# Optimization experiments

Measured on AMD Instinct MI355X. Metric: run time of the kernel, lower is better.

## Reference

```python
import jax, jax.numpy as jnp
import numpy as np

DIM = 768
HEADS = 12
HIDDEN = 3072  # int(dim * 4.0)
EPS = 1e-5


def layernorm(x, g, b):
    mu = jnp.mean(x, axis=-1, keepdims=True)
    var = jnp.mean(jnp.square(x - mu), axis=-1, keepdims=True)
    return (x - mu) * jax.lax.rsqrt(var + EPS) * g + b


def setup_inputs() -> dict:
    key = jax.random.key(0)
    ks = jax.random.split(key, 8)
    s = 0.02
    return {
        "x": jax.random.normal(ks[0], (16, 1024, DIM), dtype=jnp.float32),
        "ln1_g": jnp.ones((DIM,), jnp.float32),
        "ln1_b": jnp.zeros((DIM,), jnp.float32),
        "qkv_w": jax.random.normal(ks[1], (3 * DIM, DIM), jnp.float32) * s,  # torch Linear weight [out,in], no bias (qkv_bias=False)
        "proj_w": jax.random.normal(ks[2], (DIM, DIM), jnp.float32) * s,
        "proj_b": jnp.zeros((DIM,), jnp.float32),
        "ln2_g": jnp.ones((DIM,), jnp.float32),
        "ln2_b": jnp.zeros((DIM,), jnp.float32),
        "fc1_w": jax.random.normal(ks[3], (HIDDEN, DIM), jnp.float32) * s,
        "fc1_b": jnp.zeros((HIDDEN,), jnp.float32),
        "fc2_w": jax.random.normal(ks[4], (DIM, HIDDEN), jnp.float32) * s,
        "fc2_b": jnp.zeros((DIM,), jnp.float32),
    }


def block(x, ln1_g, ln1_b, qkv_w, proj_w, proj_b, ln2_g, ln2_b, fc1_w, fc1_b, fc2_w, fc2_b):
    B, N, C = x.shape
    hd = C // HEADS
    scale = hd ** -0.5
    # --- attention branch ---
    h = layernorm(x, ln1_g, ln1_b)
    qkv = h @ qkv_w.T                                   # [B,N,3C]
    qkv = qkv.reshape(B, N, 3, HEADS, hd)
    q, k, v = jnp.moveaxis(qkv, 2, 0)                   # each [B,N,H,hd]
    q = q.transpose(0, 2, 1, 3)                          # [B,H,N,hd]
    k = k.transpose(0, 2, 1, 3)
    v = v.transpose(0, 2, 1, 3)
    attn = jnp.einsum('bhqd,bhkd->bhqk', q, k) * scale   # [B,H,N,N]
    attn = jax.nn.softmax(attn, axis=-1)
    o = jnp.einsum('bhqk,bhkd->bhqd', attn, v)           # [B,H,N,hd]
    o = o.transpose(0, 2, 1, 3).reshape(B, N, C)
    x = x + o @ proj_w.T + proj_b
    # --- mlp branch ---
    h = layernorm(x, ln2_g, ln2_b)
    h = jax.nn.gelu(h @ fc1_w.T + fc1_b, approximate=False)
    x = x + h @ fc2_w.T + fc2_b
    return x


def reference(x, ln1_g, ln1_b, qkv_w, proj_w, proj_b, ln2_g, ln2_b, fc1_w, fc1_b, fc2_w, fc2_b):
    return block(x, ln1_g, ln1_b, qkv_w, proj_w, proj_b, ln2_g, ln2_b, fc1_w, fc1_b, fc2_w, fc2_b)
```

## Files before the change

### kernel.cpp

```cpp
#include <hip/hip_runtime.h>
#include <cstdint>
#include <cstddef>

typedef __attribute__((ext_vector_type(8))) short short8;
typedef __attribute__((ext_vector_type(4))) float f32x4;
typedef __attribute__((ext_vector_type(4))) unsigned short us4;

#define GAS(p) ((const __attribute__((address_space(1))) void*)(p))
#define LAS(p) ((__attribute__((address_space(3))) void*)(p))

__device__ __forceinline__ unsigned short f2bf(float f) {
  union { float f; unsigned u; } v; v.f = f;
  return (unsigned short)((v.u + 0x7fffu + ((v.u >> 16) & 1u)) >> 16);
}

__global__ __launch_bounds__(256) void cvt_kernel(const float* __restrict__ in,
                                                  unsigned short* __restrict__ out, int n4) {
  int i = blockIdx.x * 256 + threadIdx.x;
  if (i >= n4) return;
  f32x4 v = ((const f32x4*)in)[i];
  us4 o;
#pragma unroll
  for (int j = 0; j < 4; ++j) o[j] = f2bf(v[j]);
  ((us4*)out)[i] = o;
}

__global__ __launch_bounds__(256) void ln_kernel(const float* __restrict__ x,
                                                 const float* __restrict__ g,
                                                 const float* __restrict__ b,
                                                 unsigned short* __restrict__ out) {
  const int wave = threadIdx.x >> 6, lane = threadIdx.x & 63;
  const int row = blockIdx.x * 4 + wave;
  const float* xr = x + (size_t)row * 768;
  f32x4 v[3];
  float s = 0.f, sq = 0.f;
#pragma unroll
  for (int c = 0; c < 3; ++c) {
    v[c] = *(const f32x4*)(xr + c * 256 + lane * 4);
#pragma unroll
    for (int j = 0; j < 4; ++j) { s += v[c][j]; sq += v[c][j] * v[c][j]; }
  }
#pragma unroll
  for (int off = 32; off > 0; off >>= 1) { s += __shfl_xor(s, off); sq += __shfl_xor(sq, off); }
  const float mu = s * (1.f / 768.f);
  const float var = sq * (1.f / 768.f) - mu * mu;
  const float rs = rsqrtf(var + 1e-5f);
  unsigned short* orow = out + (size_t)row * 768;
#pragma unroll
  for (int c = 0; c < 3; ++c) {
    f32x4 gg = *(const f32x4*)(g + c * 256 + lane * 4);
    f32x4 bb = *(const f32x4*)(b + c * 256 + lane * 4);
    us4 o;
#pragma unroll
    for (int j = 0; j < 4; ++j) o[j] = f2bf((v[c][j] - mu) * rs * gg[j] + bb[j]);
    *(us4*)(orow + c * 256 + lane * 4) = o;
  }
}

template <int EPI, int NN, int K>
__global__ __launch_bounds__(1024, 4) void gemmW(
    const unsigned short* __restrict__ A, const unsigned short* __restrict__ W,
    float* __restrict__ outF, const float* __restrict__ bias, const float* __restrict__ res,
    unsigned short* __restrict__ outU,
    unsigned short* __restrict__ q, unsigned short* __restrict__ kk, unsigned short* __restrict__ vt) {
  __shared__ unsigned short As[4][8192];
  __shared__ unsigned short Bs[4][8192];
  const int tid = threadIdx.x;
  const int wave = tid >> 6, lane = tid & 63;
  const int lr = lane & 15, lg = lane >> 4;
  const int wr = wave >> 2, wc = wave & 3;
  constexpr int GX = NN / 256;
  constexpr int NWG = GX * 64;
  int id = blockIdx.y * GX + blockIdx.x;
  id = (id & 7) * (NWG / 8) + (id >> 3);
  const int row0 = (id / GX) * 256, col0 = (id % GX) * 256;
  f32x4 acc[4][4] = {};
  const int sc = ((tid & 3) ^ ((tid >> 3) & 3)) * 8;
  const unsigned short* ag = A + (size_t)(row0 + (tid >> 2)) * K + sc;
  const unsigned short* bg = W + (size_t)(col0 + (tid >> 2)) * K + sc;
  const int rsw = (lg ^ ((lr >> 1) & 3)) << 4;
  constexpr int KT = K / 32;

#define STG(buf, t_)                                                                           \
  {                                                                                            \
    __builtin_amdgcn_global_load_lds(GAS(ag + (t_) * 32), LAS(&As[buf][wave * 512]), 16, 0, 0);\
    __builtin_amdgcn_global_load_lds(GAS(bg + (t_) * 32), LAS(&Bs[buf][wave * 512]), 16, 0, 0);\
  }

#define TILE(buf, t_)                                                                          \
  {                                                                                            \
    if ((t_) < KT - 2)       { asm volatile("s_waitcnt vmcnt(4)" ::: "memory"); }              \
    else if ((t_) == KT - 2) { asm volatile("s_waitcnt vmcnt(2)" ::: "memory"); }              \
    else                     { asm volatile("s_waitcnt vmcnt(0)" ::: "memory"); }              \
    __builtin_amdgcn_s_barrier();                                                              \
    if ((t_) + 3 < KT) STG(((buf) + 3) & 3, (t_) + 3);                                         \
    const char* Ab = (const char*)As + (buf) * 16384;                                          \
    const char* Bb = (const char*)Bs + (buf) * 16384;                                          \
    short8 af[4], bfv[4];                                                                      \
    _Pragma("unroll")                                                                          \
    for (int m = 0; m < 4; ++m) {                                                              \
      const int arow = wr * 64 + m * 16 + lr;                                                  \
      af[m] = *(const short8*)(Ab + arow * 64 + rsw);                                          \
    }                                                                                          \
    _Pragma("unroll")                                                                          \
    for (int n = 0; n < 4; ++n) {                                                              \
      const int brow = wc * 64 + n * 16 + lr;                                                  \
      bfv[n] = *(const short8*)(Bb + brow * 64 + rsw);                                         \
    }                                                                                          \
    __builtin_amdgcn_s_setprio(1);                                                             \
    _Pragma("unroll")                                                                          \
    for (int m = 0; m < 4; ++m)                                                                \
      _Pragma("unroll")                                                                        \
      for (int n = 0; n < 4; ++n)                                                              \
        acc[m][n] = __builtin_amdgcn_mfma_f32_16x16x32_bf16(af[m], bfv[n], acc[m][n], 0, 0, 0);\
    __builtin_amdgcn_s_setprio(0);                                                             \
  }

  STG(0, 0);
  STG(1, 1);
  STG(2, 2);
  for (int tt = 0; tt < KT; tt += 4) {
    TILE(0, tt);
    TILE(1, tt + 1);
    TILE(2, tt + 2);
    TILE(3, tt + 3);
  }
#undef TILE
#undef STG

  if (EPI == 0) {
    const int s = (col0 >= 1536) ? 2 : (col0 >= 768 ? 1 : 0);
    const int hh = (col0 + wc * 64 - s * 768) >> 6;
#pragma unroll
    for (int m = 0; m < 4; ++m)
#pragma unroll
      for (int n = 0; n < 4; ++n) {
        const int d = n * 16 + lr;
        const int g0 = row0 + wr * 64 + m * 16 + lg * 4;
        const int bt = g0 >> 10, nt0 = g0 & 1023;
        const size_t bh = (size_t)(bt * 12 + hh);
        if (s == 2) {
          us4 o;
#pragma unroll
          for (int r = 0; r < 4; ++r) o[r] = f2bf(acc[m][n][r]);
          *(us4*)(vt + (bh * 64 + d) * 1024 + nt0) = o;
        } else {
#pragma unroll
          for (int r = 0; r < 4; ++r) {
            const float val = acc[m][n][r];
            if (s == 0) q[(bh * 1024 + nt0 + r) * 64 + d] = f2bf(val * 0.18033688f);
            else        kk[(bh * 1024 + nt0 + r) * 64 + d] = f2bf(val);
          }
        }
      }
  } else if (EPI == 1) {
#pragma unroll
    for (int m = 0; m < 4; ++m)
#pragma unroll
      for (int n = 0; n < 4; ++n) {
        const int gcol = col0 + wc * 64 + n * 16 + lr;
        const float bn = bias[gcol];
#pragma unroll
        for (int r = 0; r < 4; ++r) {
          const int grow = row0 + wr * 64 + m * 16 + lg * 4 + r;
          const size_t idx = (size_t)grow * NN + gcol;
          outF[idx] = acc[m][n][r] + bn + res[idx];
        }
      }
  } else {
#pragma unroll
    for (int m = 0; m < 4; ++m)
#pragma unroll
      for (int n = 0; n < 4; ++n) {
        const int gcol = col0 + wc * 64 + n * 16 + lr;
        const float bn = bias[gcol];
#pragma unroll
        for (int r = 0; r < 4; ++r) {
          const int grow = row0 + wr * 64 + m * 16 + lg * 4 + r;
          const size_t idx = (size_t)grow * NN + gcol;
          const float t = acc[m][n][r] + bn;
          const float u = t * (1.59576912f + t * t * 0.07135481f);
          const float eu = __expf(-u);
          outU[idx] = f2bf(t / (1.f + eu));
        }
      }
  }
}

__global__ __launch_bounds__(256) void attn_kernel(
    const unsigned short* __restrict__ Q, const unsigned short* __restrict__ K,
    const unsigned short* __restrict__ V, unsigned short* __restrict__ O) {
  __shared__ unsigned short Ks[2][64 * 64];
  __shared__ unsigned short Vs[2][64 * 64];
  __shared__ unsigned short Ps[4][32 * 64];
  const int tid = threadIdx.x, wave = tid >> 6, lane = tid & 63;
  const int lr = lane & 15, lg = lane >> 4;
  const int id = blockIdx.x;
  const int qt = (id >> 3) & 7;
  const int head = (id & 7) + 8 * (id >> 6);
  const int hh = head % 12, bb = head / 12;
  const size_t bh = (size_t)bb * 12 + hh;
  const unsigned short* Qg = Q + bh * 1024 * 64;
  const unsigned short* Kg = K + bh * 1024 * 64;
  const unsigned short* Vg = V + bh * 64 * 1024;
  const int q0 = qt * 128 + wave * 32;
  short8 aq[2][2];
#pragma unroll
  for (int nq = 0; nq < 2; ++nq)
#pragma unroll
    for (int kb = 0; kb < 2; ++kb)
      aq[nq][kb] = *(const short8*)(Qg + (size_t)(q0 + nq * 16 + lr) * 64 + kb * 32 + lg * 8);
  float m_run[2] = {-1e30f, -1e30f}, l_run[2] = {0.f, 0.f};
  f32x4 oacc[4][2] = {};
  const int srow = tid >> 3;
  const int sswz = (((tid & 7) * 16) ^ ((srow & 7) << 4)) >> 1;
  char* Pw = (char*)&Ps[wave][0];

#define ATTN_STAGE(buf, t_)                                                                      \
  {                                                                                              \
    const int kv_ = (t_) * 64;                                                                   \
    _Pragma("unroll")                                                                            \
    for (int is = 0; is < 2; ++is) {                                                             \
      __builtin_amdgcn_global_load_lds(GAS(Kg + (size_t)(kv_ + is * 32 + srow) * 64 + sswz),     \
                                       LAS(&Ks[buf][is * 2048 + wave * 512]), 16, 0, 0);         \
      __builtin_amdgcn_global_load_lds(GAS(Vg + (size_t)(is * 32 + srow) * 1024 + kv_ + sswz),   \
                                       LAS(&Vs[buf][is * 2048 + wave * 512]), 16, 0, 0);         \
    }                                                                                            \
  }

#define ATILE(cur, t_)                                                                           \
  {                                                                                              \
    if ((t_) < 15) { asm volatile("s_waitcnt vmcnt(4)" ::: "memory"); }                          \
    else           { asm volatile("s_waitcnt vmcnt(0)" ::: "memory"); }                          \
    __builtin_amdgcn_s_barrier();                                                                \
    __builtin_amdgcn_sched_barrier(0);                                                           \
    f32x4 sacc[4][2] = {};                                                                       \
    _Pragma("unroll")                                                                            \
    for (int kb = 0; kb < 2; ++kb) {                                                             \
      short8 kf[4];                                                                              \
      _Pragma("unroll")                                                                          \
      for (int mk = 0; mk < 4; ++mk) {                                                           \
        const int row = mk * 16 + lr;                                                            \
        const int boff = row * 128 + ((kb * 64 + lg * 16) ^ ((row & 7) << 4));                   \
        kf[mk] = *(const short8*)((const char*)&Ks[cur][0] + boff);                              \
      }                                                                                          \
      _Pragma("unroll")                                                                          \
      for (int mk = 0; mk < 4; ++mk)                                                             \
        _Pragma("unroll")                                                                        \
        for (int nq = 0; nq < 2; ++nq)                                                           \
          sacc[mk][nq] = __builtin_amdgcn_mfma_f32_16x16x32_bf16(kf[mk], aq[nq][kb], sacc[mk][nq], 0, 0, 0); \
    }                                                                                            \
    _Pragma("unroll")                                                                            \
    for (int nq = 0; nq < 2; ++nq) {                                                             \
      float mx = fmaxf(fmaxf(sacc[0][nq][0], sacc[0][nq][1]), fmaxf(sacc[0][nq][2], sacc[0][nq][3])); \
      _Pragma("unroll")                                                                          \
      for (int mk = 1; mk < 4; ++mk)                                                             \
        mx = fmaxf(mx, fmaxf(fmaxf(sacc[mk][nq][0], sacc[mk][nq][1]), fmaxf(sacc[mk][nq][2], sacc[mk][nq][3]))); \
      mx = fmaxf(mx, __shfl_xor(mx, 16));                                                        \
      mx = fmaxf(mx, __shfl_xor(mx, 32));                                                        \
      if (!__all(mx - m_run[nq] <= 8.f)) {                                                       \
        const float mnew = fmaxf(m_run[nq], mx);                                                 \
        const float alpha = exp2f(m_run[nq] - mnew);                                             \
        l_run[nq] *= alpha;                                                                      \
        _Pragma("unroll")                                                                        \
        for (int mb = 0; mb < 4; ++mb)                                                           \
          _Pragma("unroll")                                                                      \
          for (int r = 0; r < 4; ++r) oacc[mb][nq][r] *= alpha;                                  \
        m_run[nq] = mnew;                                                                        \
      }                                                                                          \
      float ssum = 0.f;                                                                          \
      _Pragma("unroll")                                                                          \
      for (int mk = 0; mk < 4; ++mk)                                                             \
        _Pragma("unroll")                                                                        \
        for (int r = 0; r < 4; ++r) {                                                            \
          const float p = exp2f(sacc[mk][nq][r] - m_run[nq]);                                    \
          sacc[mk][nq][r] = p;                                                                   \
          ssum += p;                                                                             \
        }                                                                                        \
      ssum += __shfl_xor(ssum, 16);                                                              \
      ssum += __shfl_xor(ssum, 32);                                                              \
      l_run[nq] += ssum;                                                                         \
      const int prow = nq * 16 + lr;                                                             \
      _Pragma("unroll")                                                                          \
      for (int mk = 0; mk < 4; ++mk) {                                                           \
        unsigned p0, p1;                                                                         \
        asm("v_cvt_pk_bf16_f32 %0, %1, %2" : "=v"(p0) : "v"(sacc[mk][nq][0]), "v"(sacc[mk][nq][1])); \
        asm("v_cvt_pk_bf16_f32 %0, %1, %2" : "=v"(p1) : "v"(sacc[mk][nq][2]), "v"(sacc[mk][nq][3])); \
        uint2 w; w.x = p0; w.y = p1;                                                             \
        *(uint2*)(Pw + prow * 128 + ((mk * 32 + lg * 8) ^ ((lr & 7) << 4))) = w;                 \
      }                                                                                          \
    }                                                                                            \
    _Pragma("unroll")                                                                            \
    for (int kb = 0; kb < 2; ++kb) {                                                             \
      short8 vf[4];                                                                              \
      _Pragma("unroll")                                                                          \
      for (int mb = 0; mb < 4; ++mb) {                                                           \
        const int row = mb * 16 + lr;                                                            \
        const int boff = row * 128 + ((kb * 64 + lg * 16) ^ ((row & 7) << 4));                   \
        vf[mb] = *(const short8*)((const char*)&Vs[cur][0] + boff);                              \
      }                                                                                          \
      _Pragma("unroll")                                                                          \
      for (int nq = 0; nq < 2; ++nq) {                                                           \
        const int prow = nq * 16 + lr;                                                           \
        const short8 pb = *(const short8*)(Pw + prow * 128 + ((kb * 64 + lg * 16) ^ ((lr & 7) << 4))); \
        _Pragma("unroll")                                                                        \
        for (int mb = 0; mb < 4; ++mb)                                                           \
          oacc[mb][nq] = __builtin_amdgcn_mfma_f32_16x16x32_bf16(vf[mb], pb, oacc[mb][nq], 0, 0, 0); \
      }                                                                                          \
    }                                                                                            \
    asm volatile("s_waitcnt lgkmcnt(0)" ::: "memory");                                           \
    __builtin_amdgcn_sched_barrier(0);                                                           \
    __builtin_amdgcn_s_barrier();                                                                \
    if ((t_) + 2 < 16) ATTN_STAGE(cur, (t_) + 2);                                                \
  }

  ATTN_STAGE(0, 0);
  ATTN_STAGE(1, 1);
  for (int tt = 0; tt < 8; ++tt) {
    ATILE(0, 2 * tt)
    ATILE(1, 2 * tt + 1)
  }
#undef ATILE
#undef ATTN_STAGE
#pragma unroll
  for (int nq = 0; nq < 2; ++nq) {
    const float linv = 1.f / l_run[nq];
    const size_t tok = (size_t)(bb << 10) + q0 + nq * 16 + lr;
#pragma unroll
    for (int mb = 0; mb < 4; ++mb) {
      us4 o;
#pragma unroll
      for (int r = 0; r < 4; ++r) o[r] = f2bf(oacc[mb][nq][r] * linv);
      *(us4*)(O + tok * 768 + hh * 64 + mb * 16 + lg * 4) = o;
    }
  }
}

extern "C" void kernel_launch(void* const* d_in, const int* in_sizes, int n_in,
                              void* d_out, int out_size, void* d_ws, size_t ws_size,
                              hipStream_t stream) {
  const float* x      = (const float*)d_in[0];
  const float* ln1_g  = (const float*)d_in[1];
  const float* ln1_b  = (const float*)d_in[2];
  const float* qkv_w  = (const float*)d_in[3];
  const float* proj_w = (const float*)d_in[4];
  const float* proj_b = (const float*)d_in[5];
  const float* ln2_g  = (const float*)d_in[6];
  const float* ln2_b  = (const float*)d_in[7];
  const float* fc1_w  = (const float*)d_in[8];
  const float* fc1_b  = (const float*)d_in[9];
  const float* fc2_w  = (const float*)d_in[10];
  const float* fc2_b  = (const float*)d_in[11];
  float* out = (float*)d_out;
  char* ws = (char*)d_ws;

  unsigned short* wqkv = (unsigned short*)(ws + 0);
  unsigned short* wproj = (unsigned short*)(ws + 3538944);
  unsigned short* wfc1 = (unsigned short*)(ws + 4718592);
  unsigned short* wfc2 = (unsigned short*)(ws + 9437184);
  unsigned short* hbuf = (unsigned short*)(ws + 14155776);
  char* big = ws + 39321600;
  unsigned short* qb  = (unsigned short*)(big);
  unsigned short* kb  = (unsigned short*)(big + 25165824);
  unsigned short* vtb = (unsigned short*)(big + 50331648);
  unsigned short* ob  = (unsigned short*)(big + 75497472);
  unsigned short* hid = (unsigned short*)(big);

  cvt_kernel<<<1728, 256, 0, stream>>>(qkv_w, wqkv, 442368);
  cvt_kernel<<<576, 256, 0, stream>>>(proj_w, wproj, 147456);
  cvt_kernel<<<2304, 256, 0, stream>>>(fc1_w, wfc1, 589824);
  cvt_kernel<<<2304, 256, 0, stream>>>(fc2_w, wfc2, 589824);

  ln_kernel<<<4096, 256, 0, stream>>>(x, ln1_g, ln1_b, hbuf);
  gemmW<0, 2304, 768><<<dim3(9, 64), 1024, 0, stream>>>(
      hbuf, wqkv, nullptr, nullptr, nullptr, nullptr, qb, kb, vtb);
  attn_kernel<<<dim3(1536), 256, 0, stream>>>(qb, kb, vtb, ob);
  gemmW<1, 768, 768><<<dim3(3, 64), 1024, 0, stream>>>(
      ob, wproj, out, proj_b, x, nullptr, nullptr, nullptr, nullptr);
  ln_kernel<<<4096, 256, 0, stream>>>(out, ln2_g, ln2_b, hbuf);
  gemmW<2, 3072, 768><<<dim3(12, 64), 1024, 0, stream>>>(
      hbuf, wfc1, nullptr, fc1_b, nullptr, hid, nullptr, nullptr, nullptr);
  gemmW<1, 768, 3072><<<dim3(3, 64), 1024, 0, stream>>>(
      hid, wfc2, out, fc2_b, out, nullptr, nullptr, nullptr, nullptr);
}
```

Before: 462.6 us.

## Parameterize GEMM tile width and compute softmax row sums via MFMA

The GEMM kernel gets a templated N-tile width (BN). The QKV, proj and fc2 GEMMs switch to 192-wide tiles, giving more workgroups (768 or 256 instead of 576 or 192) for better CU fill on the 256-CU part, and the B-tile load wraps rows when BN<256. In attention, the per-row exp-sum with cross-lane shuffles is replaced by an extra MFMA against a vector of bf16 ones, and the max reduction is restructured into a chain. The cost is an extra MFMA per block, and the bf16-rounded P now also feeds the denominator, which slightly changes numerics.

```diff
diff --git a/kernel.cpp b/kernel.cpp
--- a/kernel.cpp
+++ b/kernel.cpp
@@ -57,34 +57,38 @@
   }
 }
 
-template <int EPI, int NN, int K>
+template <int EPI, int NN, int K, int BN>
 __global__ __launch_bounds__(1024, 4) void gemmW(
     const unsigned short* __restrict__ A, const unsigned short* __restrict__ W,
     float* __restrict__ outF, const float* __restrict__ bias, const float* __restrict__ res,
     unsigned short* __restrict__ outU,
     unsigned short* __restrict__ q, unsigned short* __restrict__ kk, unsigned short* __restrict__ vt) {
+  constexpr int NFR = BN / 64;
+  constexpr int BW = BN >> 4;
   __shared__ unsigned short As[4][8192];
-  __shared__ unsigned short Bs[4][8192];
+  __shared__ unsigned short Bs[4][BN * 32];
   const int tid = threadIdx.x;
   const int wave = tid >> 6, lane = tid & 63;
   const int lr = lane & 15, lg = lane >> 4;
   const int wr = wave >> 2, wc = wave & 3;
-  constexpr int GX = NN / 256;
+  constexpr int GX = NN / BN;
   constexpr int NWG = GX * 64;
   int id = blockIdx.y * GX + blockIdx.x;
   id = (id & 7) * (NWG / 8) + (id >> 3);
-  const int row0 = (id / GX) * 256, col0 = (id % GX) * 256;
-  f32x4 acc[4][4] = {};
+  const int row0 = (id / GX) * 256, col0 = (id % GX) * BN;
+  f32x4 acc[4][NFR] = {};
   const int sc = ((tid & 3) ^ ((tid >> 3) & 3)) * 8;
+  int br = tid >> 2; if (br >= BN) br -= BN;
   const unsigned short* ag = A + (size_t)(row0 + (tid >> 2)) * K + sc;
-  const unsigned short* bg = W + (size_t)(col0 + (tid >> 2)) * K + sc;
+  const unsigned short* bg = W + (size_t)(col0 + br) * K + sc;
+  const int bwav = (wave < BW ? wave : wave - BW) * 512;
   const int rsw = (lg ^ ((lr >> 1) & 3)) << 4;
   constexpr int KT = K / 32;
 
 #define STG(buf, t_)                                                                           \
   {                                                                                            \
     __builtin_amdgcn_global_load_lds(GAS(ag + (t_) * 32), LAS(&As[buf][wave * 512]), 16, 0, 0);\
-    __builtin_amdgcn_global_load_lds(GAS(bg + (t_) * 32), LAS(&Bs[buf][wave * 512]), 16, 0, 0);\
+    __builtin_amdgcn_global_load_lds(GAS(bg + (t_) * 32), LAS(&Bs[buf][bwav]), 16, 0, 0);      \
   }
 
 #define TILE(buf, t_)                                                                          \
@@ -95,23 +99,23 @@
     __builtin_amdgcn_s_barrier();                                                              \
     if ((t_) + 3 < KT) STG(((buf) + 3) & 3, (t_) + 3);                                         \
     const char* Ab = (const char*)As + (buf) * 16384;                                          \
-    const char* Bb = (const char*)Bs + (buf) * 16384;                                          \
-    short8 af[4], bfv[4];                                                                      \
+    const char* Bb = (const char*)&Bs[buf][0];                                                 \
+    short8 af[4], bfv[NFR];                                                                    \
     _Pragma("unroll")                                                                          \
     for (int m = 0; m < 4; ++m) {                                                              \
       const int arow = wr * 64 + m * 16 + lr;                                                  \
       af[m] = *(const short8*)(Ab + arow * 64 + rsw);                                          \
     }                                                                                          \
     _Pragma("unroll")                                                                          \
-    for (int n = 0; n < 4; ++n) {                                                              \
-      const int brow = wc * 64 + n * 16 + lr;                                                  \
+    for (int n = 0; n < NFR; ++n) {                                                            \
+      const int brow = wc * (NFR * 16) + n * 16 + lr;                                          \
       bfv[n] = *(const short8*)(Bb + brow * 64 + rsw);                                         \
     }                                                                                          \
     __builtin_amdgcn_s_setprio(1);                                                             \
     _Pragma("unroll")                                                                          \
     for (int m = 0; m < 4; ++m)                                                                \
       _Pragma("unroll")                                                                        \
-      for (int n = 0; n < 4; ++n)                                                              \
+      for (int n = 0; n < NFR; ++n)                                                            \
         acc[m][n] = __builtin_amdgcn_mfma_f32_16x16x32_bf16(af[m], bfv[n], acc[m][n], 0, 0, 0);\
     __builtin_amdgcn_s_setprio(0);                                                             \
   }
@@ -130,12 +134,13 @@
 
   if (EPI == 0) {
     const int s = (col0 >= 1536) ? 2 : (col0 >= 768 ? 1 : 0);
-    const int hh = (col0 + wc * 64 - s * 768) >> 6;
 #pragma unroll
     for (int m = 0; m < 4; ++m)
 #pragma unroll
-      for (int n = 0; n < 4; ++n) {
-        const int d = n * 16 + lr;
+      for (int n = 0; n < NFR; ++n) {
+        const int gb = col0 - s * 768 + wc * (NFR * 16) + n * 16;
+        const int hh = gb >> 6;
+        const int d = (gb & 63) + lr;
         const int g0 = row0 + wr * 64 + m * 16 + lg * 4;
         const int bt = g0 >> 10, nt0 = g0 & 1023;
         const size_t bh = (size_t)(bt * 12 + hh);
@@ -157,8 +162,8 @@
 #pragma unroll
     for (int m = 0; m < 4; ++m)
 #pragma unroll
-      for (int n = 0; n < 4; ++n) {
-        const int gcol = col0 + wc * 64 + n * 16 + lr;
+      for (int n = 0; n < NFR; ++n) {
+        const int gcol = col0 + wc * (NFR * 16) + n * 16 + lr;
         const float bn = bias[gcol];
 #pragma unroll
         for (int r = 0; r < 4; ++r) {
@@ -171,8 +176,8 @@
 #pragma unroll
     for (int m = 0; m < 4; ++m)
 #pragma unroll
-      for (int n = 0; n < 4; ++n) {
-        const int gcol = col0 + wc * 64 + n * 16 + lr;
+      for (int n = 0; n < NFR; ++n) {
+        const int gcol = col0 + wc * (NFR * 16) + n * 16 + lr;
         const float bn = bias[gcol];
 #pragma unroll
         for (int r = 0; r < 4; ++r) {
@@ -210,8 +215,12 @@
 #pragma unroll
     for (int kb = 0; kb < 2; ++kb)
       aq[nq][kb] = *(const short8*)(Qg + (size_t)(q0 + nq * 16 + lr) * 64 + kb * 32 + lg * 8);
-  float m_run[2] = {-1e30f, -1e30f}, l_run[2] = {0.f, 0.f};
+  float m_run[2] = {-1e30f, -1e30f};
   f32x4 oacc[4][2] = {};
+  f32x4 accl[2] = {};
+  short8 vones;
+#pragma unroll
+  for (int j = 0; j < 8; ++j) vones[j] = (short)0x3F80;
   const int srow = tid >> 3;
   const int sswz = (((tid & 7) * 16) ^ ((srow & 7) << 4)) >> 1;
   char* Pw = (char*)&Ps[wave][0];
@@ -252,34 +261,31 @@
     }                                                                                            \
     _Pragma("unroll")                                                                            \
     for (int nq = 0; nq < 2; ++nq) {                                                             \
-      float mx = fmaxf(fmaxf(sacc[0][nq][0], sacc[0][nq][1]), fmaxf(sacc[0][nq][2], sacc[0][nq][3])); \
-      _Pragma("unroll")                                                                          \
-      for (int mk = 1; mk < 4; ++mk)                                                             \
-        mx = fmaxf(mx, fmaxf(fmaxf(sacc[mk][nq][0], sacc[mk][nq][1]), fmaxf(sacc[mk][nq][2], sacc[mk][nq][3]))); \
+      float mx = fmaxf(fmaxf(sacc[0][nq][0], sacc[0][nq][1]), sacc[0][nq][2]);                   \
+      mx = fmaxf(fmaxf(mx, sacc[0][nq][3]), sacc[1][nq][0]);                                     \
+      mx = fmaxf(fmaxf(mx, sacc[1][nq][1]), sacc[1][nq][2]);                                     \
+      mx = fmaxf(fmaxf(mx, sacc[1][nq][3]), sacc[2][nq][0]);                                     \
+      mx = fmaxf(fmaxf(mx, sacc[2][nq][1]), sacc[2][nq][2]);                                     \
+      mx = fmaxf(fmaxf(mx, sacc[2][nq][3]), sacc[3][nq][0]);                                     \
+      mx = fmaxf(fmaxf(mx, sacc[3][nq][1]), sacc[3][nq][2]);                                     \
+      mx = fmaxf(mx, sacc[3][nq][3]);                                                            \
       mx = fmaxf(mx, __shfl_xor(mx, 16));                                                        \
       mx = fmaxf(mx, __shfl_xor(mx, 32));                                                        \
       if (!__all(mx - m_run[nq] <= 8.f)) {                                                       \
         const float mnew = fmaxf(m_run[nq], mx);                                                 \
         const float alpha = exp2f(m_run[nq] - mnew);                                             \
-        l_run[nq] *= alpha;                                                                      \
+        accl[nq][0] *= alpha; accl[nq][1] *= alpha; accl[nq][2] *= alpha; accl[nq][3] *= alpha;  \
         _Pragma("unroll")                                                                        \
         for (int mb = 0; mb < 4; ++mb)                                                           \
           _Pragma("unroll")                                                                      \
           for (int r = 0; r < 4; ++r) oacc[mb][nq][r] *= alpha;                                  \
         m_run[nq] = mnew;                                                                        \
       }                                                                                          \
-      float ssum = 0.f;                                                                          \
       _Pragma("unroll")                                                                          \
       for (int mk = 0; mk < 4; ++mk)                                                             \
         _Pragma("unroll")                                                                        \
-        for (int r = 0; r < 4; ++r) {                                                            \
-          const float p = exp2f(sacc[mk][nq][r] - m_run[nq]);                                    \
-          sacc[mk][nq][r] = p;                                                                   \
-          ssum += p;                                                                             \
-        }                                                                                        \
-      ssum += __shfl_xor(ssum, 16);                                                              \
-      ssum += __shfl_xor(ssum, 32);                                                              \
-      l_run[nq] += ssum;                                                                         \
+        for (int r = 0; r < 4; ++r)                                                              \
+          sacc[mk][nq][r] = exp2f(sacc[mk][nq][r] - m_run[nq]);                                  \
       const int prow = nq * 16 + lr;                                                             \
       _Pragma("unroll")                                                                          \
       for (int mk = 0; mk < 4; ++mk) {                                                           \
@@ -303,6 +309,7 @@
       for (int nq = 0; nq < 2; ++nq) {                                                           \
         const int prow = nq * 16 + lr;                                                           \
         const short8 pb = *(const short8*)(Pw + prow * 128 + ((kb * 64 + lg * 16) ^ ((lr & 7) << 4))); \
+        accl[nq] = __builtin_amdgcn_mfma_f32_16x16x32_bf16(vones, pb, accl[nq], 0, 0, 0);        \
         _Pragma("unroll")                                                                        \
         for (int mb = 0; mb < 4; ++mb)                                                           \
           oacc[mb][nq] = __builtin_amdgcn_mfma_f32_16x16x32_bf16(vf[mb], pb, oacc[mb][nq], 0, 0, 0); \
@@ -324,7 +331,7 @@
 #undef ATTN_STAGE
 #pragma unroll
   for (int nq = 0; nq < 2; ++nq) {
-    const float linv = 1.f / l_run[nq];
+    const float linv = 1.f / accl[nq][0];
     const size_t tok = (size_t)(bb << 10) + q0 + nq * 16 + lr;
 #pragma unroll
     for (int mb = 0; mb < 4; ++mb) {
@@ -372,14 +379,14 @@
   cvt_kernel<<<2304, 256, 0, stream>>>(fc2_w, wfc2, 589824);
 
   ln_kernel<<<4096, 256, 0, stream>>>(x, ln1_g, ln1_b, hbuf);
-  gemmW<0, 2304, 768><<<dim3(9, 64), 1024, 0, stream>>>(
+  gemmW<0, 2304, 768, 192><<<dim3(12, 64), 1024, 0, stream>>>(
       hbuf, wqkv, nullptr, nullptr, nullptr, nullptr, qb, kb, vtb);
   attn_kernel<<<dim3(1536), 256, 0, stream>>>(qb, kb, vtb, ob);
-  gemmW<1, 768, 768><<<dim3(3, 64), 1024, 0, stream>>>(
+  gemmW<1, 768, 768, 192><<<dim3(4, 64), 1024, 0, stream>>>(
       ob, wproj, out, proj_b, x, nullptr, nullptr, nullptr, nullptr);
   ln_kernel<<<4096, 256, 0, stream>>>(out, ln2_g, ln2_b, hbuf);
-  gemmW<2, 3072, 768><<<dim3(12, 64), 1024, 0, stream>>>(
+  gemmW<2, 3072, 768, 256><<<dim3(12, 64), 1024, 0, stream>>>(
       hbuf, wfc1, nullptr, fc1_b, nullptr, hid, nullptr, nullptr, nullptr);
-  gemmW<1, 768, 3072><<<dim3(3, 64), 1024, 0, stream>>>(
+  gemmW<1, 768, 3072, 192><<<dim3(4, 64), 1024, 0, stream>>>(
       hid, wfc2, out, fc2_b, out, nullptr, nullptr, nullptr, nullptr);
 }
```

Result: faster. 452.5 us (-2.2%).
